# Kernel tuning notes

Measured on AMD Instinct MI355X. Metric: run time of the kernel, lower is better.

## Reference

```python
import jax, jax.numpy as jnp
import numpy as np
from jax import lax

RATIOS = [0.5, 1.0, 2.0]
SCALES = [8, 16, 32]
BASE = 16
FEAT_STRIDE = 16
NMS_THRESH = 0.7
PRE_NMS = 2000
POST_NMS = 300
MIN_SIZE = 16.0
SCALE = 1.0
A = len(RATIOS) * len(SCALES)  # 9


def _anchor_base():
    ab = []
    py = px = BASE / 2.0
    for r in RATIOS:
        for s in SCALES:
            h = BASE * s * np.sqrt(r)
            w = BASE * s * np.sqrt(1.0 / r)
            ab.append([py - h / 2.0, px - w / 2.0, py + h / 2.0, px + w / 2.0])
    return jnp.asarray(np.array(ab, dtype=np.float32))  # (A,4)


def _shifted_anchors(H, W):
    base = _anchor_base()
    sy = jnp.arange(H, dtype=jnp.float32) * FEAT_STRIDE
    sx = jnp.arange(W, dtype=jnp.float32) * FEAT_STRIDE
    gy, gx = jnp.meshgrid(sy, sx, indexing='ij')
    shift = jnp.stack([gy.ravel(), gx.ravel(), gy.ravel(), gx.ravel()], axis=1)  # (K,4)
    return (shift[:, None, :] + base[None, :, :]).reshape(-1, 4)  # (K*A,4)


def _conv(x, w, b, pad):
    y = lax.conv_general_dilated(x, w, (1, 1), ((pad, pad), (pad, pad)),
                                 dimension_numbers=('NCHW', 'OIHW', 'NCHW'))
    return y + b[None, :, None, None]


def _loc2bbox(anchor, loc):
    h = anchor[:, 2] - anchor[:, 0]
    w = anchor[:, 3] - anchor[:, 1]
    cy = anchor[:, 0] + 0.5 * h
    cx = anchor[:, 1] + 0.5 * w
    dy, dx, dh, dw = loc[:, 0], loc[:, 1], loc[:, 2], loc[:, 3]
    ncy = dy * h + cy
    ncx = dx * w + cx
    nh = jnp.exp(dh) * h
    nw = jnp.exp(dw) * w
    return jnp.stack([ncy - 0.5 * nh, ncx - 0.5 * nw, ncy + 0.5 * nh, ncx + 0.5 * nw], axis=1)


def _iou_matrix(b):
    area = (b[:, 2] - b[:, 0]) * (b[:, 3] - b[:, 1])
    ty = jnp.maximum(b[:, None, 0], b[None, :, 0])
    tx = jnp.maximum(b[:, None, 1], b[None, :, 1])
    by = jnp.minimum(b[:, None, 2], b[None, :, 2])
    bx = jnp.minimum(b[:, None, 3], b[None, :, 3])
    inter = jnp.maximum(by - ty, 0.0) * jnp.maximum(bx - tx, 0.0)
    return inter / (area[:, None] + area[None, :] - inter)


def _proposals(loc_i, fg_i, anchor, img_h, img_w):
    boxes = _loc2bbox(anchor, loc_i)
    boxes = jnp.stack([
        jnp.clip(boxes[:, 0], 0.0, float(img_h)),
        jnp.clip(boxes[:, 1], 0.0, float(img_w)),
        jnp.clip(boxes[:, 2], 0.0, float(img_h)),
        jnp.clip(boxes[:, 3], 0.0, float(img_w)),
    ], axis=1)
    hs = boxes[:, 2] - boxes[:, 0]
    ws = boxes[:, 3] - boxes[:, 1]
    valid = (hs >= MIN_SIZE * SCALE) & (ws >= MIN_SIZE * SCALE)
    sc = jnp.where(valid, fg_i, -jnp.inf)
    top_sc, idx = lax.top_k(sc, PRE_NMS)          # sorted by score desc
    b = boxes[idx]                                # (PRE_NMS,4)
    iou = _iou_matrix(b)                          # (PRE_NMS,PRE_NMS)
    rng = jnp.arange(PRE_NMS)

    def body(i, keep):
        sup = (iou[i] > NMS_THRESH) & keep[i] & (rng > i)
        return keep & ~sup

    keep = lax.fori_loop(0, PRE_NMS, body, top_sc > -jnp.inf)
    order = jnp.argsort(jnp.where(keep, rng, PRE_NMS))  # kept indices first, score order
    sel = order[:POST_NMS]
    n_keep = jnp.sum(keep)
    valid_out = jnp.arange(POST_NMS) < n_keep
    rois = jnp.where(valid_out[:, None], b[sel], 0.0)
    return rois, valid_out


def setup_inputs() -> dict:
    key = jax.random.key(0)
    ks = jax.random.split(key, 4)
    return {
        'x': jax.random.normal(ks[0], (4, 1024, 64, 64), dtype=jnp.float32),
        'conv1_w': 0.01 * jax.random.normal(ks[1], (512, 1024, 3, 3), dtype=jnp.float32),
        'conv1_b': jnp.zeros((512,), dtype=jnp.float32),
        'score_w': 0.01 * jax.random.normal(ks[2], (18, 512, 1, 1), dtype=jnp.float32),
        'score_b': jnp.zeros((18,), dtype=jnp.float32),
        'loc_w': 0.01 * jax.random.normal(ks[3], (36, 512, 1, 1), dtype=jnp.float32),
        'loc_b': jnp.zeros((36,), dtype=jnp.float32),
        'img_h': 1024,
        'img_w': 1024,
    }


def reference(x, conv1_w, conv1_b, score_w, score_b, loc_w, loc_b, img_h, img_w):
    n, _, H, W = x.shape
    anchor = _shifted_anchors(H, W)                       # (HWA,4)
    mid = jax.nn.relu(_conv(x, conv1_w, conv1_b, 1))
    rpn_locs = _conv(mid, loc_w, loc_b, 0).transpose(0, 2, 3, 1).reshape(n, -1, 4)
    rpn_scores = _conv(mid, score_w, score_b, 0).transpose(0, 2, 3, 1)
    soft = jax.nn.softmax(rpn_scores.reshape(n, H, W, A, 2), axis=4)
    rpn_fg = soft[..., 1].reshape(n, -1)
    rpn_scores = rpn_scores.reshape(n, -1, 2)
    rois, valid = jax.vmap(lambda l, s: _proposals(l, s, anchor, img_h, img_w))(rpn_locs, rpn_fg)
    roi_indices = jnp.where(valid, jnp.arange(n, dtype=jnp.int32)[:, None], -1)
    return (rpn_locs, rpn_scores, rois.reshape(-1, 4), roi_indices.reshape(-1), anchor)
```

## Files before the change

kernel.cpp:

```cpp
#include <hip/hip_runtime.h>
#include <math.h>

#define NIMG 4
#define CIN 1024
#define CMID 512
#define HGT 64
#define WID 64
#define NA 9
#define NPOS 36864
#define PRE 2000
#define POST 300
#define CBLK 4

#define LOCOFF   0
#define SCOREOFF 589824
#define ROISOFF  884736
#define RIDXOFF  889536
#define ANCHOFF  890736

typedef __attribute__((address_space(1))) const void glob_cv;
typedef __attribute__((address_space(3))) void lds_v;

__global__ __launch_bounds__(256) void wtrans_kernel(
    const float* __restrict__ w, double* __restrict__ wt64)
{
    __shared__ float ts[64][65];
    const int t = threadIdx.x;
    const int rt0 = blockIdx.x * 64;
    const int ct0 = blockIdx.y * 64;
    const int j = t & 63;
    const int i0 = t >> 6;
#pragma unroll
    for (int k = 0; k < 16; ++k) {
        int i = i0 + k * 4;
        ts[i][j] = w[(size_t)(ct0 + i) * (CIN * 9) + rt0 + j];
    }
    __syncthreads();
    const int cout = ct0 + j;
    const size_t blk = (size_t)(cout >> 5) * (9216 * 32) + (cout & 31);
#pragma unroll
    for (int k = 0; k < 16; ++k) {
        int jj = i0 + k * 4;
        wt64[blk + (size_t)(rt0 + jj) * 32] = (double)ts[j][jj];
    }
}

__global__ __launch_bounds__(256) void conv1_kernel(
    const float* __restrict__ x, const double* __restrict__ wt64,
    const float* __restrict__ bias, float* __restrict__ mid)
{
    __shared__ __align__(16) float  Xl[2][CBLK][6][64];
    __shared__ __align__(16) double Wl[2][CBLK][9][32];
    const int t = threadIdx.x;
    const int rowgrp = blockIdx.x, coutgrp = blockIdx.y, img = blockIdx.z;
    const int y0 = rowgrp * 4, c0 = coutgrp * 32;
    const int pg = t & 7, cg = (t >> 3) & 7, rowi = t >> 6;
    const int p0 = pg * 8, cc0 = cg * 4;
    const int lane = t & 63;

    if (rowgrp == 0) {
        for (int i = t; i < 2 * CBLK * 64; i += 256) {
            int b = i / (CBLK * 64), rem = i % (CBLK * 64);
            Xl[b][rem >> 6][0][rem & 63] = 0.f;
        }
    }
    if (rowgrp == 15) {
        for (int i = t; i < 2 * CBLK * 64; i += 256) {
            int b = i / (CBLK * 64), rem = i % (CBLK * 64);
            Xl[b][rem >> 6][5][rem & 63] = 0.f;
        }
    }

    const int rlo = (rowgrp == 0) ? 1 : 0;
    const int rhi = (rowgrp == 15) ? 4 : 5;
    const int nrows = rhi - rlo + 1;
    const double* wslab = wt64 + (size_t)coutgrp * (9216 * 32);

    auto issue = [&](int ci0, int nb) {
        int nx = CBLK * nrows;
        for (int k = rowi; k < nx; k += 4) {
            int cl = k / nrows, row = rlo + k % nrows;
            int gr = y0 - 1 + row;
            const float* gp =
                &x[(((size_t)img * CIN + ci0 + cl) * HGT + gr) * WID] + lane;
            __builtin_amdgcn_global_load_lds(
                (glob_cv*)gp, (lds_v*)&Xl[nb][cl][row][0], 4, 0, 0);
        }
        const double* wb = wslab + (size_t)ci0 * (9 * 32);
        double* ldsw = &Wl[nb][0][0][0];
        for (int k = rowi; k < 9; k += 4) {
            const double* gp = wb + k * 128 + lane * 2;
            __builtin_amdgcn_global_load_lds(
                (glob_cv*)gp, (lds_v*)(ldsw + k * 128), 16, 0, 0);
        }
    };

    double acc[8][4];
#pragma unroll
    for (int i = 0; i < 8; ++i)
#pragma unroll
        for (int c = 0; c < 4; ++c) acc[i][c] = 0.0;

    issue(0, 0);

#pragma unroll 1
    for (int s = 0; s < 256; ++s) {
        const int buf = s & 1;
        __syncthreads();
        if (s < 255) issue((s + 1) * CBLK, buf ^ 1);

#pragma unroll 1
        for (int cl = 0; cl < CBLK; ++cl) {
#pragma unroll
            for (int dy = 0; dy < 3; ++dy) {
                const float* xr = &Xl[buf][cl][rowi + dy][0];
                float f0 = (pg != 0) ? xr[p0 - 1] : 0.f;
                float4 xa = *(const float4*)(xr + p0);
                float4 xb = *(const float4*)(xr + p0 + 4);
                float f9 = (pg != 7) ? xr[p0 + 8] : 0.f;
                double xd[10];
                xd[0] = (double)f0;
                xd[1] = (double)xa.x; xd[2] = (double)xa.y;
                xd[3] = (double)xa.z; xd[4] = (double)xa.w;
                xd[5] = (double)xb.x; xd[6] = (double)xb.y;
                xd[7] = (double)xb.z; xd[8] = (double)xb.w;
                xd[9] = (double)f9;
#pragma unroll
                for (int dx = 0; dx < 3; ++dx) {
                    const double* wp = &Wl[buf][cl][dy * 3 + dx][cc0];
                    double2 wa = *(const double2*)(wp);
                    double2 wb2 = *(const double2*)(wp + 2);
                    double w0 = wa.x, w1 = wa.y, w2 = wb2.x, w3 = wb2.y;
#pragma unroll
                    for (int i = 0; i < 8; ++i) {
                        double xv = xd[i + dx];
                        acc[i][0] += xv * w0;
                        acc[i][1] += xv * w1;
                        acc[i][2] += xv * w2;
                        acc[i][3] += xv * w3;
                    }
                }
            }
        }
    }

#pragma unroll
    for (int co = 0; co < 4; ++co) {
        double bb = (double)bias[c0 + cc0 + co];
        float tmp[8];
#pragma unroll
        for (int i = 0; i < 8; ++i) {
            double v = acc[i][co] + bb;
            v = v > 0.0 ? v : 0.0;
            tmp[i] = (float)v;
        }
        float* dst = &mid[((img * CMID + c0 + cc0 + co) * HGT + (y0 + rowi)) * WID + p0];
        *(float4*)dst = make_float4(tmp[0], tmp[1], tmp[2], tmp[3]);
        *(float4*)(dst + 4) = make_float4(tmp[4], tmp[5], tmp[6], tmp[7]);
    }
}

__global__ __launch_bounds__(256) void conv1x1_kernel(
    const float* __restrict__ mid,
    const float* __restrict__ sw, const float* __restrict__ sb,
    const float* __restrict__ lw, const float* __restrict__ lb,
    float* __restrict__ out, double* __restrict__ locws, double* __restrict__ keyws)
{
    const int t = threadIdx.x;
    const int p = blockIdx.x * 256 + t;
    const int g = blockIdx.y;
    const int img = blockIdx.z;

    double acc[14];
#pragma unroll
    for (int k = 0; k < 14; ++k) acc[k] = 0.0;

    const float* mp = &mid[(size_t)img * CMID * 4096 + p];
    for (int cin = 0; cin < CMID; ++cin) {
        double xd = (double)mp[(size_t)cin * 4096];
#pragma unroll
        for (int k = 0; k < 14; ++k) {
            int c = g * 14 + k;
            double wv = 0.0;
            if (c < 36)      wv = (double)lw[c * CMID + cin];
            else if (c < 54) wv = (double)sw[(c - 36) * CMID + cin];
            acc[k] += xd * wv;
        }
    }

    double prev = 0.0;
#pragma unroll
    for (int k = 0; k < 14; ++k) {
        int c = g * 14 + k;
        if (c >= 54) continue;
        if (c < 36) {
            double v = acc[k] + (double)lb[c];
            int a = c >> 2, cc = c & 3;
            size_t ix = (size_t)img * NPOS + (size_t)p * NA + a;
            locws[ix * 4 + cc] = v;
            out[LOCOFF + ix * 4 + cc] = (float)v;
        } else {
            int sc = c - 36;
            double v = acc[k] + (double)sb[sc];
            int a = sc >> 1;
            size_t ix = (size_t)img * NPOS + (size_t)p * NA + a;
            out[SCOREOFF + ix * 2 + (sc & 1)] = (float)v;
            if (sc & 1) keyws[ix] = v - prev;
            prev = v;
        }
    }
}

__device__ __forceinline__ unsigned mono_of(double k) {
    unsigned fb = __float_as_uint((float)k);
    return (fb & 0x80000000u) ? ~fb : (fb | 0x80000000u);
}

__global__ __launch_bounds__(256) void boxes_kernel(
    double* __restrict__ keyio, const double* __restrict__ locws,
    const int* __restrict__ imh, const int* __restrict__ imw,
    float* __restrict__ out, double* __restrict__ boxes, unsigned* __restrict__ hist)
{
    __shared__ unsigned lh[4096];
    const int t = threadIdx.x;
    const int img = blockIdx.y;
    const int pos = blockIdx.x * 256 + t;
    for (int i = t; i < 4096; i += 256) lh[i] = 0;
    __syncthreads();

    int a = pos % 9, hw = pos / 9;
    int hy = hw >> 6, hx = hw & 63;
    int r_idx = a / 3, s_idx = a % 3;
    double ratio = r_idx == 0 ? 0.5 : (r_idx == 1 ? 1.0 : 2.0);
    double scl   = s_idx == 0 ? 8.0 : (s_idx == 1 ? 16.0 : 32.0);
    double hh2 = 8.0 * scl * sqrt(ratio);
    double ww2 = 8.0 * scl * sqrt(1.0 / ratio);
    float ay1 = (float)(8.0 - hh2), ax1 = (float)(8.0 - ww2);
    float ay2 = (float)(8.0 + hh2), ax2 = (float)(8.0 + ww2);
    float sy = (float)(hy * 16), sx = (float)(hx * 16);
    float A0 = sy + ay1, A1 = sx + ax1, A2 = sy + ay2, A3 = sx + ax2;
    if (img == 0) {
        size_t ao = ANCHOFF + (size_t)pos * 4;
        out[ao + 0] = A0; out[ao + 1] = A1; out[ao + 2] = A2; out[ao + 3] = A3;
    }

    size_t ix = (size_t)img * NPOS + pos;
    const double* lp = &locws[ix * 4];
    double h = (double)A2 - (double)A0, w_ = (double)A3 - (double)A1;
    double cy = (double)A0 + 0.5 * h, cx = (double)A1 + 0.5 * w_;
    double dy = lp[0], dx = lp[1], dh = lp[2], dw = lp[3];
    double ncy = dy * h + cy, ncx = dx * w_ + cx;
    double nh = exp(dh) * h, nw = exp(dw) * w_;
    double Hc = (double)imh[0], Wc = (double)imw[0];
    double y1 = ncy - 0.5 * nh, x1 = ncx - 0.5 * nw;
    double y2 = ncy + 0.5 * nh, x2 = ncx + 0.5 * nw;
    y1 = fmin(fmax(y1, 0.0), Hc); x1 = fmin(fmax(x1, 0.0), Wc);
    y2 = fmin(fmax(y2, 0.0), Hc); x2 = fmin(fmax(x2, 0.0), Wc);
    boxes[ix * 4 + 0] = y1; boxes[ix * 4 + 1] = x1;
    boxes[ix * 4 + 2] = y2; boxes[ix * 4 + 3] = x2;

    bool valid = ((y2 - y1) >= 16.0) && ((x2 - x1) >= 16.0);
    double kg = valid ? keyio[ix] : -INFINITY;
    keyio[ix] = kg;
    atomicAdd(&lh[mono_of(kg) >> 20], 1u);
    __syncthreads();
    for (int i = t; i < 4096; i += 256)
        if (lh[i]) atomicAdd(&hist[img * 4096 + i], lh[i]);
}

__global__ void cutoff_kernel(const unsigned* __restrict__ hist, int* __restrict__ cutoffb)
{
    if (threadIdx.x) return;
    int img = blockIdx.x;
    unsigned cum = 0; int cb = 0;
    for (int b = 4095; b >= 0; --b) {
        cum += hist[img * 4096 + b];
        if (cum >= PRE) { cb = b; break; }
    }
    cutoffb[img] = cb;
}

__global__ __launch_bounds__(256) void compact_kernel(
    const double* __restrict__ keyio, const int* __restrict__ cutoffb,
    int* __restrict__ candCnt, int* __restrict__ candIdx, double* __restrict__ candKey)
{
    int img = blockIdx.y;
    int pos = blockIdx.x * 256 + threadIdx.x;
    size_t ix = (size_t)img * NPOS + pos;
    double k = keyio[ix];
    if ((int)(mono_of(k) >> 20) >= cutoffb[img]) {
        int p = atomicAdd(&candCnt[img], 1);
        candIdx[img * NPOS + p] = pos;
        candKey[(size_t)img * NPOS + p] = k;
    }
}

__global__ __launch_bounds__(256) void rank_kernel(
    const int* __restrict__ candCnt, const int* __restrict__ candIdx,
    const double* __restrict__ candKey, const double* __restrict__ boxes,
    int* __restrict__ topIdx, int* __restrict__ topValid, double* __restrict__ bsel)
{
    __shared__ double sk[256];
    __shared__ int si[256];
    int img = blockIdx.y, t = threadIdx.x;
    int M = candCnt[img];
    if (blockIdx.x * 256 >= M) return;
    int i = blockIdx.x * 256 + t;
    bool act = i < M;
    double ki = 0.0; int pi = 0;
    if (act) { ki = candKey[(size_t)img * NPOS + i]; pi = candIdx[img * NPOS + i]; }
    int rank = 0;
    for (int jb = 0; jb < M; jb += 256) {
        int j = jb + t;
        if (j < M) { sk[t] = candKey[(size_t)img * NPOS + j]; si[t] = candIdx[img * NPOS + j]; }
        __syncthreads();
        int lim = min(256, M - jb);
        if (act) {
            for (int jj = 0; jj < lim; ++jj) {
                double kj = sk[jj]; int pj = si[jj];
                rank += (kj > ki || (kj == ki && pj < pi)) ? 1 : 0;
            }
        }
        __syncthreads();
    }
    if (act && rank < PRE) {
        topIdx[img * PRE + rank] = pi;
        topValid[img * PRE + rank] = (ki != -INFINITY) ? 1 : 0;
        const double* bp = &boxes[((size_t)img * NPOS + pi) * 4];
        double* bs = &bsel[((size_t)img * PRE + rank) * 4];
        bs[0] = bp[0]; bs[1] = bp[1]; bs[2] = bp[2]; bs[3] = bp[3];
    }
}

__global__ __launch_bounds__(256) void mask_kernel(
    const double* __restrict__ bsel, unsigned long long* __restrict__ mask)
{
    int i = blockIdx.x, img = blockIdx.y, t = threadIdx.x;
    const double* bi = &bsel[((size_t)img * PRE + i) * 4];
    double y1i = bi[0], x1i = bi[1], y2i = bi[2], x2i = bi[3];
    double ai = (y2i - y1i) * (x2i - x1i);
#pragma unroll 1
    for (int it = 0; it < 8; ++it) {
        int j = it * 256 + t;
        bool pred = false;
        if (j < PRE && j > i) {
            const double* bj = &bsel[((size_t)img * PRE + j) * 4];
            double ty = fmax(y1i, bj[0]), tx = fmax(x1i, bj[1]);
            double by = fmin(y2i, bj[2]), bx = fmin(x2i, bj[3]);
            double inter = fmax(by - ty, 0.0) * fmax(bx - tx, 0.0);
            double aj = (bj[2] - bj[0]) * (bj[3] - bj[1]);
            double iou = inter / (ai + aj - inter);
            pred = iou > 0.7;
        }
        unsigned long long m = __ballot(pred);
        if ((t & 63) == 0)
            mask[((size_t)img * PRE + i) * 32 + it * 4 + (t >> 6)] = m;
    }
}

__global__ void nms_kernel(const unsigned long long* __restrict__ mask,
                           const int* __restrict__ topValid, int* __restrict__ keepA)
{
    int img = blockIdx.x, lane = threadIdx.x;
    size_t base = (size_t)img * PRE;
    unsigned long long remv = 0;
    if (lane < 32) {
        unsigned long long tv = 0;
        for (int b = 0; b < 64; ++b) {
            int idx = lane * 64 + b;
            if (idx < PRE && topValid[base + idx]) tv |= (1ull << b);
        }
        remv = ~tv;
    }
    const unsigned long long* mrow = &mask[base * 32];
    unsigned long long c0 = 0, c1 = 0, c2 = 0, c3 = 0;
    if (lane < 32) {
        c0 = mrow[(size_t)0 * 32 + lane]; c1 = mrow[(size_t)1 * 32 + lane];
        c2 = mrow[(size_t)2 * 32 + lane]; c3 = mrow[(size_t)3 * 32 + lane];
    }
    for (int i = 0; i < PRE; i += 4) {
        unsigned long long n0 = 0, n1 = 0, n2 = 0, n3 = 0;
        if (lane < 32 && i + 4 < PRE) {
            n0 = mrow[(size_t)(i + 4) * 32 + lane];
            n1 = mrow[(size_t)(i + 5) * 32 + lane];
            n2 = mrow[(size_t)(i + 6) * 32 + lane];
            n3 = mrow[(size_t)(i + 7) * 32 + lane];
        }
        {
            unsigned long long rw = __shfl(remv, i >> 6);
            int kp = !((rw >> (i & 63)) & 1ull);
            if (lane == 0) keepA[base + i] = kp;
            if (kp) remv |= c0;
        }
        {
            int ii = i + 1;
            unsigned long long rw = __shfl(remv, ii >> 6);
            int kp = !((rw >> (ii & 63)) & 1ull);
            if (lane == 0) keepA[base + ii] = kp;
            if (kp) remv |= c1;
        }
        {
            int ii = i + 2;
            unsigned long long rw = __shfl(remv, ii >> 6);
            int kp = !((rw >> (ii & 63)) & 1ull);
            if (lane == 0) keepA[base + ii] = kp;
            if (kp) remv |= c2;
        }
        {
            int ii = i + 3;
            unsigned long long rw = __shfl(remv, ii >> 6);
            int kp = !((rw >> (ii & 63)) & 1ull);
            if (lane == 0) keepA[base + ii] = kp;
            if (kp) remv |= c3;
        }
        c0 = n0; c1 = n1; c2 = n2; c3 = n3;
    }
}

__global__ __launch_bounds__(256) void final_kernel(
    const int* __restrict__ keepA, const double* __restrict__ bsel, float* __restrict__ out)
{
    __shared__ int ssum[256];
    __shared__ int stot;
    int img = blockIdx.x, t = threadIdx.x;
    size_t base = (size_t)img * PRE;
    int loc[8]; int s = 0;
#pragma unroll
    for (int k = 0; k < 8; ++k) {
        int i = t * 8 + k;
        loc[k] = (i < PRE) ? keepA[base + i] : 0;
        s += loc[k];
    }
    ssum[t] = s;
    __syncthreads();
    if (t == 0) {
        int run = 0;
        for (int u = 0; u < 256; ++u) { int tmp = ssum[u]; ssum[u] = run; run += tmp; }
        stot = run;
    }
    __syncthreads();
    int run = ssum[t];
#pragma unroll
    for (int k = 0; k < 8; ++k) {
        int i = t * 8 + k;
        if (i < PRE && loc[k]) {
            int p = run++;
            if (p < POST) {
                const double* bp = &bsel[(base + i) * 4];
                size_t ro = ROISOFF + ((size_t)img * POST + p) * 4;
                out[ro + 0] = (float)bp[0]; out[ro + 1] = (float)bp[1];
                out[ro + 2] = (float)bp[2]; out[ro + 3] = (float)bp[3];
                out[RIDXOFF + img * POST + p] = (float)img;
            }
        }
    }
    __syncthreads();
    int nk = stot;
    for (int r = t; r < POST; r += 256) {
        if (r >= nk) {
            size_t ro = ROISOFF + ((size_t)img * POST + r) * 4;
            out[ro + 0] = 0.f; out[ro + 1] = 0.f; out[ro + 2] = 0.f; out[ro + 3] = 0.f;
            out[RIDXOFF + img * POST + r] = -1.f;
        }
    }
}

extern "C" void kernel_launch(void* const* d_in, const int* in_sizes, int n_in,
                              void* d_out, int out_size, void* d_ws, size_t ws_size,
                              hipStream_t stream)
{
    const float* x   = (const float*)d_in[0];
    const float* c1w = (const float*)d_in[1];
    const float* c1b = (const float*)d_in[2];
    const float* sw  = (const float*)d_in[3];
    const float* sb  = (const float*)d_in[4];
    const float* lw  = (const float*)d_in[5];
    const float* lb  = (const float*)d_in[6];
    const int*   ih  = (const int*)d_in[7];
    const int*   iw  = (const int*)d_in[8];
    float* out = (float*)d_out;
    (void)in_sizes; (void)n_in; (void)out_size; (void)ws_size;

    char* ws = (char*)d_ws;
    size_t off = 0;
    auto alloc = [&](size_t bytes) -> void* {
        void* p = (void*)(ws + off);
        off = (off + bytes + 255) & ~(size_t)255;
        return p;
    };
    float*  mid      = (float*) alloc((size_t)NIMG * CMID * 4096 * 4);
    double* wt64     = (double*)alloc((size_t)CMID * CIN * 9 * 8);
    double* locws    = (double*)alloc((size_t)NIMG * NPOS * 4 * 8);
    double* keyws    = (double*)alloc((size_t)NIMG * NPOS * 8);
    double* boxes    = (double*)alloc((size_t)NIMG * NPOS * 4 * 8);
    unsigned* hist   = (unsigned*)alloc((size_t)NIMG * 4096 * 4);
    int*    cutoffb  = (int*)   alloc(64);
    int*    candCnt  = (int*)   alloc(64);
    int*    candIdx  = (int*)   alloc((size_t)NIMG * NPOS * 4);
    double* candKey  = (double*)alloc((size_t)NIMG * NPOS * 8);
    int*    topIdx   = (int*)   alloc((size_t)NIMG * PRE * 4);
    int*    topValid = (int*)   alloc((size_t)NIMG * PRE * 4);
    double* bsel     = (double*)alloc((size_t)NIMG * PRE * 4 * 8);
    unsigned long long* mask = (unsigned long long*)alloc((size_t)NIMG * PRE * 32 * 8);
    int*    keepA    = (int*)   alloc((size_t)NIMG * PRE * 4);

    hipMemsetAsync(hist, 0, (size_t)NIMG * 4096 * 4, stream);
    hipMemsetAsync(candCnt, 0, 64, stream);

    wtrans_kernel <<<dim3(144, 8),       256, 0, stream>>>(c1w, wt64);
    conv1_kernel  <<<dim3(16, 16, NIMG), 256, 0, stream>>>(x, wt64, c1b, mid);
    conv1x1_kernel<<<dim3(16, 4, NIMG),  256, 0, stream>>>(mid, sw, sb, lw, lb, out, locws, keyws);
    boxes_kernel  <<<dim3(144, NIMG),    256, 0, stream>>>(keyws, locws, ih, iw, out, boxes, hist);
    cutoff_kernel <<<NIMG, 64, 0, stream>>>(hist, cutoffb);
    compact_kernel<<<dim3(144, NIMG),    256, 0, stream>>>(keyws, cutoffb, candCnt, candIdx, candKey);
    rank_kernel   <<<dim3(144, NIMG),    256, 0, stream>>>(candCnt, candIdx, candKey, boxes,
                                                           topIdx, topValid, bsel);
    mask_kernel   <<<dim3(PRE, NIMG),    256, 0, stream>>>(bsel, mask);
    nms_kernel    <<<NIMG, 64, 0, stream>>>(mask, topValid, keepA);
    final_kernel  <<<NIMG, 256, 0, stream>>>(keepA, bsel, out);
}
```

Baseline: 4.715 ms.

## Split conv1 reduction over input channels and fuse bias/ReLU into 1x1 conv

```diff
diff --git a/kernel.cpp b/kernel.cpp
--- a/kernel.cpp
+++ b/kernel.cpp
@@ -11,6 +11,8 @@
 #define PRE 2000
 #define POST 300
 #define CBLK 4
+#define KSPLIT 2
+#define KHALF 512
 
 #define LOCOFF   0
 #define SCOREOFF 589824
@@ -47,16 +49,18 @@
 
 __global__ __launch_bounds__(256) void conv1_kernel(
     const float* __restrict__ x, const double* __restrict__ wt64,
-    const float* __restrict__ bias, float* __restrict__ mid)
+    double* __restrict__ hbuf)
 {
     __shared__ __align__(16) float  Xl[2][CBLK][6][64];
     __shared__ __align__(16) double Wl[2][CBLK][9][32];
     const int t = threadIdx.x;
-    const int rowgrp = blockIdx.x, coutgrp = blockIdx.y, img = blockIdx.z;
+    const int rowgrp = blockIdx.x, coutgrp = blockIdx.y;
+    const int img = blockIdx.z >> 1, half = blockIdx.z & 1;
     const int y0 = rowgrp * 4, c0 = coutgrp * 32;
     const int pg = t & 7, cg = (t >> 3) & 7, rowi = t >> 6;
     const int p0 = pg * 8, cc0 = cg * 4;
     const int lane = t & 63;
+    const int cin0 = half * KHALF;
 
     if (rowgrp == 0) {
         for (int i = t; i < 2 * CBLK * 64; i += 256) {
@@ -101,13 +105,13 @@
 #pragma unroll
         for (int c = 0; c < 4; ++c) acc[i][c] = 0.0;
 
-    issue(0, 0);
+    issue(cin0, 0);
 
 #pragma unroll 1
-    for (int s = 0; s < 256; ++s) {
+    for (int s = 0; s < KHALF / CBLK; ++s) {
         const int buf = s & 1;
         __syncthreads();
-        if (s < 255) issue((s + 1) * CBLK, buf ^ 1);
+        if (s < KHALF / CBLK - 1) issue(cin0 + (s + 1) * CBLK, buf ^ 1);
 
 #pragma unroll 1
         for (int cl = 0; cl < CBLK; ++cl) {
@@ -146,22 +150,16 @@
 
 #pragma unroll
     for (int co = 0; co < 4; ++co) {
-        double bb = (double)bias[c0 + cc0 + co];
-        float tmp[8];
-#pragma unroll
-        for (int i = 0; i < 8; ++i) {
-            double v = acc[i][co] + bb;
-            v = v > 0.0 ? v : 0.0;
-            tmp[i] = (float)v;
-        }
-        float* dst = &mid[((img * CMID + c0 + cc0 + co) * HGT + (y0 + rowi)) * WID + p0];
-        *(float4*)dst = make_float4(tmp[0], tmp[1], tmp[2], tmp[3]);
-        *(float4*)(dst + 4) = make_float4(tmp[4], tmp[5], tmp[6], tmp[7]);
+        double* dst = &hbuf[(((size_t)(half * NIMG + img) * CMID + c0 + cc0 + co)
+                             * 4096) + (size_t)(y0 + rowi) * 64 + p0];
+#pragma unroll
+        for (int i = 0; i < 8; i += 2)
+            *(double2*)(dst + i) = make_double2(acc[i][co], acc[i + 1][co]);
     }
 }
 
 __global__ __launch_bounds__(256) void conv1x1_kernel(
-    const float* __restrict__ mid,
+    const double* __restrict__ hbuf, const float* __restrict__ c1b,
     const float* __restrict__ sw, const float* __restrict__ sb,
     const float* __restrict__ lw, const float* __restrict__ lb,
     float* __restrict__ out, double* __restrict__ locws, double* __restrict__ keyws)
@@ -175,9 +173,13 @@
 #pragma unroll
     for (int k = 0; k < 14; ++k) acc[k] = 0.0;
 
-    const float* mp = &mid[(size_t)img * CMID * 4096 + p];
+    const double* h1 = hbuf + (size_t)img * CMID * 4096 + p;
+    const double* h2 = hbuf + (size_t)(NIMG + img) * CMID * 4096 + p;
     for (int cin = 0; cin < CMID; ++cin) {
-        double xd = (double)mp[(size_t)cin * 4096];
+        double m = h1[(size_t)cin * 4096] + h2[(size_t)cin * 4096]
+                   + (double)c1b[cin];
+        m = m > 0.0 ? m : 0.0;
+        double xd = (double)(float)m;
 #pragma unroll
         for (int k = 0; k < 14; ++k) {
             int c = g * 14 + k;
@@ -488,7 +490,7 @@
         off = (off + bytes + 255) & ~(size_t)255;
         return p;
     };
-    float*  mid      = (float*) alloc((size_t)NIMG * CMID * 4096 * 4);
+    double* hbuf     = (double*)alloc((size_t)KSPLIT * NIMG * CMID * 4096 * 8);
     double* wt64     = (double*)alloc((size_t)CMID * CIN * 9 * 8);
     double* locws    = (double*)alloc((size_t)NIMG * NPOS * 4 * 8);
     double* keyws    = (double*)alloc((size_t)NIMG * NPOS * 8);
@@ -507,15 +509,16 @@
     hipMemsetAsync(hist, 0, (size_t)NIMG * 4096 * 4, stream);
     hipMemsetAsync(candCnt, 0, 64, stream);
 
-    wtrans_kernel <<<dim3(144, 8),       256, 0, stream>>>(c1w, wt64);
-    conv1_kernel  <<<dim3(16, 16, NIMG), 256, 0, stream>>>(x, wt64, c1b, mid);
-    conv1x1_kernel<<<dim3(16, 4, NIMG),  256, 0, stream>>>(mid, sw, sb, lw, lb, out, locws, keyws);
-    boxes_kernel  <<<dim3(144, NIMG),    256, 0, stream>>>(keyws, locws, ih, iw, out, boxes, hist);
+    wtrans_kernel <<<dim3(144, 8),              256, 0, stream>>>(c1w, wt64);
+    conv1_kernel  <<<dim3(16, 16, NIMG * KSPLIT), 256, 0, stream>>>(x, wt64, hbuf);
+    conv1x1_kernel<<<dim3(16, 4, NIMG),         256, 0, stream>>>(hbuf, c1b, sw, sb, lw, lb,
+                                                                  out, locws, keyws);
+    boxes_kernel  <<<dim3(144, NIMG),           256, 0, stream>>>(keyws, locws, ih, iw, out, boxes, hist);
     cutoff_kernel <<<NIMG, 64, 0, stream>>>(hist, cutoffb);
-    compact_kernel<<<dim3(144, NIMG),    256, 0, stream>>>(keyws, cutoffb, candCnt, candIdx, candKey);
-    rank_kernel   <<<dim3(144, NIMG),    256, 0, stream>>>(candCnt, candIdx, candKey, boxes,
-                                                           topIdx, topValid, bsel);
-    mask_kernel   <<<dim3(PRE, NIMG),    256, 0, stream>>>(bsel, mask);
+    compact_kernel<<<dim3(144, NIMG),           256, 0, stream>>>(keyws, cutoffb, candCnt, candIdx, candKey);
+    rank_kernel   <<<dim3(144, NIMG),           256, 0, stream>>>(candCnt, candIdx, candKey, boxes,
+                                                                  topIdx, topValid, bsel);
+    mask_kernel   <<<dim3(PRE, NIMG),           256, 0, stream>>>(bsel, mask);
     nms_kernel    <<<NIMG, 64, 0, stream>>>(mask, topValid, keepA);
     final_kernel  <<<NIMG, 256, 0, stream>>>(keepA, bsel, out);
 }
```

New measurement: 4.660 ms. About the same (-1.2%).
